# Kernel tuning notes

Measured on AMD Instinct MI355X. Metric: run time of the kernel, lower is better.

The kernel has to match this reference:

```python
import jax, jax.numpy as jnp
import numpy as np

G = 128            # grid_size (hardcoded in NeRFRenderer.__init__)
T = 32             # time_size (reduced from 64 to keep working set < 4GB)
CAS = 1            # cascade = 1 + ceil(log2(bound)), bound = 1
DECAY = 0.95
DENSITY_SCALE = 1.0
DENSITY_THRESH = 0.01


def _expand_bits(v):
    # instant-ngp style 10-bit -> 30-bit expansion (works for 7-bit coords of G=128)
    v = (v * jnp.uint32(0x00010001)) & jnp.uint32(0xFF0000FF)
    v = (v * jnp.uint32(0x00000101)) & jnp.uint32(0x0F00F00F)
    v = (v * jnp.uint32(0x00000011)) & jnp.uint32(0xC30C30C3)
    v = (v * jnp.uint32(0x00000005)) & jnp.uint32(0x49249249)
    return v


def _morton3d(coords):
    # coords: [N, 3] int32 in [0, G)
    x = _expand_bits(coords[:, 0].astype(jnp.uint32))
    y = _expand_bits(coords[:, 1].astype(jnp.uint32))
    z = _expand_bits(coords[:, 2].astype(jnp.uint32))
    return (x | (y << 1) | (z << 2)).astype(jnp.int32)


def setup_inputs() -> dict:
    key = jax.random.key(0)
    k1, k2 = jax.random.split(key)
    density_grid = jax.random.normal(k1, (T, CAS, G ** 3), dtype=jnp.float32) * 0.5
    sigmas = jax.random.uniform(k2, (T, CAS, G ** 3), dtype=jnp.float32)
    return {"density_grid": density_grid, "sigmas": sigmas}


def reference(density_grid, sigmas):
    # full-grid branch of update_extra_state (iter_density < 16)
    g = jnp.arange(G, dtype=jnp.int32)
    xx, yy, zz = jnp.meshgrid(g, g, g, indexing='ij')
    coords = jnp.stack([xx.ravel(), yy.ravel(), zz.ravel()], axis=-1)  # [G^3, 3]
    indices = _morton3d(coords)                                        # [G^3]

    # tmp_grid = -1; tmp_grid[t, cas, indices] = sigmas * density_scale
    tmp_grid = -jnp.ones_like(density_grid)
    tmp_grid = tmp_grid.at[:, :, indices].set(sigmas * DENSITY_SCALE)

    # decay / max merge on mutually-valid cells
    valid = (density_grid >= 0) & (tmp_grid >= 0)
    new_grid = jnp.where(valid, jnp.maximum(density_grid * DECAY, tmp_grid), density_grid)

    # threshold + packbits into bitfield (8 cells per byte, morton order)
    mean_density = jnp.mean(jnp.clip(new_grid, 0.0))
    thresh = jnp.minimum(mean_density, jnp.float32(DENSITY_THRESH))
    bits = (new_grid > thresh).reshape(T, -1, 8)                       # [T, CAS*G^3/8, 8]
    weights = (jnp.int32(1) << jnp.arange(8, dtype=jnp.int32))
    bitfield = jnp.sum(bits.astype(jnp.int32) * weights, axis=-1)      # [T, CAS*G^3/8]
    return new_grid, bitfield
```

## Files before the change

kernel.cpp:

```cpp
#include <hip/hip_runtime.h>

#define G    128
#define G3   (G * G * G)
#define TDIM 32
#define NTOT (TDIM * G3)
#define NBYTES_OUT (NTOT / 8)
#define DECAY 0.95f
#define DTH   0.01f
#define NBLK  (TDIM * 256)

typedef float f32x4 __attribute__((ext_vector_type(4)));
typedef float f32x2 __attribute__((ext_vector_type(2)));

__device__ __forceinline__ unsigned expand3(unsigned v) {
    v = (v * 0x00010001u) & 0xFF0000FFu;
    v = (v * 0x00000101u) & 0x0F00F00Fu;
    v = (v * 0x00000011u) & 0xC30C30C3u;
    v = (v * 0x00000005u) & 0x49249249u;
    return v;
}

__device__ __forceinline__ int swz(int f) {
    return f ^ ((((f >> 12) & 1) << 3) ^ (((f >> 8) & 1) << 4));
}

__device__ __forceinline__ f32x4 merge4(f32x4 v, f32x4 s) {
    f32x4 r;
    r.x = (v.x >= 0.f && s.x >= 0.f) ? fmaxf(v.x * DECAY, s.x) : v.x;
    r.y = (v.y >= 0.f && s.y >= 0.f) ? fmaxf(v.y * DECAY, s.y) : v.y;
    r.z = (v.z >= 0.f && s.z >= 0.f) ? fmaxf(v.z * DECAY, s.z) : v.z;
    r.w = (v.w >= 0.f && s.w >= 0.f) ? fmaxf(v.w * DECAY, s.w) : v.w;
    return r;
}

__global__ __launch_bounds__(512, 8) void
pass1(const float* __restrict__ dg, const float* __restrict__ sg,
      float* __restrict__ out_grid, float* __restrict__ out_bits,
      float* __restrict__ partials)
{
    __shared__ float smem[8192];
    __shared__ float wsum[8];
    const int blk  = blockIdx.x;
    const int t    = blk >> 8;
    const int pp   = blk & 255;
    const int sx   = pp & 15;
    const int sy   = pp >> 4;
    const int base = t * G3;
    const int tid  = threadIdx.x;

    const int m_fixed = (int)((expand3((unsigned)sx) << 9) | (expand3((unsigned)sy) << 10));
    const int r   = tid >> 5;
    const int o   = (tid & 31) << 4;
    const int jg0 = base + m_fixed + (int)(expand3((unsigned)r) << 11) + o;

    const f32x4* dgp = reinterpret_cast<const f32x4*>(dg + jg0);
    const f32x4 v0 = dgp[0];
    const f32x4 v1 = dgp[1];
    const f32x4 v2 = dgp[2];
    const f32x4 v3 = dgp[3];

    const float* __restrict__ sgt = sg + base + (sx << 17) + (sy << 10);
    #pragma unroll
    for (int k = 0; k < 4; ++k) {
        const int c   = tid + (k << 9);
        const int x   = c >> 8;
        const int rem = c & 255;
        const f32x4 s = *reinterpret_cast<const f32x4*>(sgt + (x << 14) + (rem << 2));
        *reinterpret_cast<f32x4*>(&smem[swz((x << 10) + (rem << 2))]) = s;
    }
    __syncthreads();

    const int lb = tid & 31;
    const int y1 = lb & 1, z1 = (lb >> 1) & 1, x2 = (lb >> 2) & 1;
    const int y2 = (lb >> 3) & 1, z2 = (lb >> 4) & 1;
    const int zz = (z1 << 1) + (z2 << 2) + (r << 3);

    f32x2 p0, p1, p2, p3, p4, p5, p6, p7;
    {
        const int xA = 2 * 0 + 4 * x2;
        const int xB = 2 * 1 + 4 * x2;
        const int yA = 2 * y1 + 4 * y2;
        const int fA = (xA << 10) + (yA << 7) + zz;
        const int fB = (xB << 10) + (yA << 7) + zz;
        p0 = *reinterpret_cast<const f32x2*>(&smem[swz(fA)]);
        p1 = *reinterpret_cast<const f32x2*>(&smem[swz(fA + 1024)]);
        p2 = *reinterpret_cast<const f32x2*>(&smem[swz(fA + 128)]);
        p3 = *reinterpret_cast<const f32x2*>(&smem[swz(fA + 1152)]);
        p4 = *reinterpret_cast<const f32x2*>(&smem[swz(fB)]);
        p5 = *reinterpret_cast<const f32x2*>(&smem[swz(fB + 1024)]);
        p6 = *reinterpret_cast<const f32x2*>(&smem[swz(fB + 128)]);
        p7 = *reinterpret_cast<const f32x2*>(&smem[swz(fB + 1152)]);
    }
    f32x4 s0; s0.x = p0.x; s0.y = p1.x; s0.z = p2.x; s0.w = p3.x;
    f32x4 s1; s1.x = p0.y; s1.y = p1.y; s1.z = p2.y; s1.w = p3.y;
    f32x4 s2; s2.x = p4.x; s2.y = p5.x; s2.z = p6.x; s2.w = p7.x;
    f32x4 s3; s3.x = p4.y; s3.y = p5.y; s3.z = p6.y; s3.w = p7.y;

    const f32x4 r0 = merge4(v0, s0);
    const f32x4 r1 = merge4(v1, s1);
    const f32x4 r2 = merge4(v2, s2);
    const f32x4 r3 = merge4(v3, s3);

    f32x4* ogp = reinterpret_cast<f32x4*>(out_grid + jg0);
    ogp[0] = r0;
    ogp[1] = r1;
    ogp[2] = r2;
    ogp[3] = r3;

    float lsum = fmaxf(r0.x, 0.f) + fmaxf(r0.y, 0.f) + fmaxf(r0.z, 0.f) + fmaxf(r0.w, 0.f)
               + fmaxf(r1.x, 0.f) + fmaxf(r1.y, 0.f) + fmaxf(r1.z, 0.f) + fmaxf(r1.w, 0.f)
               + fmaxf(r2.x, 0.f) + fmaxf(r2.y, 0.f) + fmaxf(r2.z, 0.f) + fmaxf(r2.w, 0.f)
               + fmaxf(r3.x, 0.f) + fmaxf(r3.y, 0.f) + fmaxf(r3.z, 0.f) + fmaxf(r3.w, 0.f);

    const int byte0 = (r0.x > DTH ? 1 : 0)  | (r0.y > DTH ? 2 : 0)  |
                      (r0.z > DTH ? 4 : 0)  | (r0.w > DTH ? 8 : 0)  |
                      (r1.x > DTH ? 16 : 0) | (r1.y > DTH ? 32 : 0) |
                      (r1.z > DTH ? 64 : 0) | (r1.w > DTH ? 128 : 0);
    const int byte1 = (r2.x > DTH ? 1 : 0)  | (r2.y > DTH ? 2 : 0)  |
                      (r2.z > DTH ? 4 : 0)  | (r2.w > DTH ? 8 : 0)  |
                      (r3.x > DTH ? 16 : 0) | (r3.y > DTH ? 32 : 0) |
                      (r3.z > DTH ? 64 : 0) | (r3.w > DTH ? 128 : 0);
    f32x2 bb; bb.x = (float)byte0; bb.y = (float)byte1;
    *reinterpret_cast<f32x2*>(out_bits + (jg0 >> 3)) = bb;

    #pragma unroll
    for (int offl = 32; offl; offl >>= 1) lsum += __shfl_down(lsum, offl, 64);
    if ((tid & 63) == 0) wsum[tid >> 6] = lsum;
    __syncthreads();
    if (tid == 0) {
        float tot = 0.f;
        #pragma unroll
        for (int i = 0; i < 8; ++i) tot += wsum[i];
        partials[blk] = tot;
    }
}

__global__ __launch_bounds__(1024) void
reduce_thresh(const float* __restrict__ partials, float* __restrict__ thresh)
{
    float s = 0.f;
    for (int i = threadIdx.x; i < NBLK; i += 1024) s += partials[i];
    #pragma unroll
    for (int off = 32; off; off >>= 1) s += __shfl_down(s, off, 64);
    __shared__ float wsum[16];
    if ((threadIdx.x & 63) == 0) wsum[threadIdx.x >> 6] = s;
    __syncthreads();
    if (threadIdx.x == 0) {
        float tot = 0.f;
        #pragma unroll
        for (int i = 0; i < 16; ++i) tot += wsum[i];
        thresh[0] = fminf(tot / (float)NTOT, DTH);
    }
}

__global__ __launch_bounds__(256) void
fix_bits(const float* __restrict__ grid, const float* __restrict__ thresh,
         float* __restrict__ out_bits)
{
    const float th = thresh[0];
    if (th == DTH) return;
    for (int n = blockIdx.x * 256 + threadIdx.x; n < NBYTES_OUT; n += 256 * 1024) {
        const float4* g = reinterpret_cast<const float4*>(grid) + (n << 1);
        const float4 a = g[0], b = g[1];
        int byte = (a.x > th ? 1 : 0)   | (a.y > th ? 2 : 0)   |
                   (a.z > th ? 4 : 0)   | (a.w > th ? 8 : 0)   |
                   (b.x > th ? 16 : 0)  | (b.y > th ? 32 : 0)  |
                   (b.z > th ? 64 : 0)  | (b.w > th ? 128 : 0);
        out_bits[n] = (float)byte;
    }
}

extern "C" void kernel_launch(void* const* d_in, const int* in_sizes, int n_in,
                              void* d_out, int out_size, void* d_ws, size_t ws_size,
                              hipStream_t stream)
{
    const float* dg = (const float*)d_in[0];
    const float* sg = (const float*)d_in[1];
    float* out_grid = (float*)d_out;
    float* out_bits = out_grid + NTOT;
    float* partials = (float*)d_ws;
    float* thresh   = partials + NBLK;

    pass1<<<NBLK, 512, 0, stream>>>(dg, sg, out_grid, out_bits, partials);
    reduce_thresh<<<1, 1024, 0, stream>>>(partials, thresh);
    fix_bits<<<1024, 256, 0, stream>>>(out_grid, thresh, out_bits);
}
```

Baseline: 160.8 us.

## Remap thread-to-cell assignment for coalesced grid access and conflict-free LDS reads

Each thread now handles four 16-byte chunks spaced 64/512/576 vectors apart instead of four contiguous vectors, so each wavefront's global loads and stores of the grid cover contiguous 1KB runs. The LDS swizzle and the gather of sigmas from shared memory are reworked to match, using scalar loads chosen to avoid bank conflicts. Bitfield bytes are built from nibbles exchanged between lane pairs with a shuffle, and only even lanes write them. The cost is extra shuffles, more scalar LDS reads and half the lanes idle during the bitfield store.

```diff
diff --git a/kernel.cpp b/kernel.cpp
--- a/kernel.cpp
+++ b/kernel.cpp
@@ -21,7 +21,7 @@
 }
 
 __device__ __forceinline__ int swz(int f) {
-    return f ^ ((((f >> 12) & 1) << 3) ^ (((f >> 8) & 1) << 4));
+    return f ^ ((((f >> 11) & 1) << 2) | (((f >> 8) & 1) << 3) | (((f >> 12) & 1) << 4));
 }
 
 __device__ __forceinline__ f32x4 merge4(f32x4 v, f32x4 s) {
@@ -47,17 +47,17 @@
     const int sy   = pp >> 4;
     const int base = t * G3;
     const int tid  = threadIdx.x;
+    const int w    = tid >> 6;
+    const int i    = tid & 63;
 
     const int m_fixed = (int)((expand3((unsigned)sx) << 9) | (expand3((unsigned)sy) << 10));
-    const int r   = tid >> 5;
-    const int o   = (tid & 31) << 4;
-    const int jg0 = base + m_fixed + (int)(expand3((unsigned)r) << 11) + o;
+    const int jgA = base + m_fixed + ((int)expand3((unsigned)w) << 14) + (i << 2);
 
-    const f32x4* dgp = reinterpret_cast<const f32x4*>(dg + jg0);
+    const f32x4* dgp = reinterpret_cast<const f32x4*>(dg + jgA);
     const f32x4 v0 = dgp[0];
-    const f32x4 v1 = dgp[1];
-    const f32x4 v2 = dgp[2];
-    const f32x4 v3 = dgp[3];
+    const f32x4 v1 = dgp[64];
+    const f32x4 v2 = dgp[512];
+    const f32x4 v3 = dgp[576];
 
     const float* __restrict__ sgt = sg + base + (sx << 17) + (sy << 10);
     #pragma unroll
@@ -70,58 +70,50 @@
     }
     __syncthreads();
 
-    const int lb = tid & 31;
-    const int y1 = lb & 1, z1 = (lb >> 1) & 1, x2 = (lb >> 2) & 1;
-    const int y2 = (lb >> 3) & 1, z2 = (lb >> 4) & 1;
-    const int zz = (z1 << 1) + (z2 << 2) + (r << 3);
-
-    f32x2 p0, p1, p2, p3, p4, p5, p6, p7;
-    {
-        const int xA = 2 * 0 + 4 * x2;
-        const int xB = 2 * 1 + 4 * x2;
-        const int yA = 2 * y1 + 4 * y2;
-        const int fA = (xA << 10) + (yA << 7) + zz;
-        const int fB = (xB << 10) + (yA << 7) + zz;
-        p0 = *reinterpret_cast<const f32x2*>(&smem[swz(fA)]);
-        p1 = *reinterpret_cast<const f32x2*>(&smem[swz(fA + 1024)]);
-        p2 = *reinterpret_cast<const f32x2*>(&smem[swz(fA + 128)]);
-        p3 = *reinterpret_cast<const f32x2*>(&smem[swz(fA + 1152)]);
-        p4 = *reinterpret_cast<const f32x2*>(&smem[swz(fB)]);
-        p5 = *reinterpret_cast<const f32x2*>(&smem[swz(fB + 1024)]);
-        p6 = *reinterpret_cast<const f32x2*>(&smem[swz(fB + 128)]);
-        p7 = *reinterpret_cast<const f32x2*>(&smem[swz(fB + 1152)]);
-    }
-    f32x4 s0; s0.x = p0.x; s0.y = p1.x; s0.z = p2.x; s0.w = p3.x;
-    f32x4 s1; s1.x = p0.y; s1.y = p1.y; s1.z = p2.y; s1.w = p3.y;
-    f32x4 s2; s2.x = p4.x; s2.y = p5.x; s2.z = p6.x; s2.w = p7.x;
-    f32x4 s3; s3.x = p4.y; s3.y = p5.y; s3.z = p6.y; s3.w = p7.y;
+    const int fi = (i & 1) | (((i >> 3) & 1) << 1) | (((i >> 2) & 1) << 8)
+                 | (((i >> 5) & 1) << 9) | (((i >> 1) & 1) << 11) | (((i >> 4) & 1) << 12);
+    const int S  = (((fi >> 11) & 1) << 2) | (((fi >> 8) & 1) << 3) | (((fi >> 12) & 1) << 4);
+    const int A  = w << 4;
+    const float* sp0 = &smem[fi | ((A + 0)  ^ S)];
+    const float* sp1 = &smem[fi | ((A + 4)  ^ S)];
+    const float* sp2 = &smem[fi | ((A + 8)  ^ S)];
+    const float* sp3 = &smem[fi | ((A + 12) ^ S)];
+    f32x4 s0; s0.x = sp0[0]; s0.y = sp0[1024]; s0.z = sp0[128]; s0.w = sp0[1152];
+    f32x4 s1; s1.x = sp1[0]; s1.y = sp1[1024]; s1.z = sp1[128]; s1.w = sp1[1152];
+    f32x4 s2; s2.x = sp2[0]; s2.y = sp2[1024]; s2.z = sp2[128]; s2.w = sp2[1152];
+    f32x4 s3; s3.x = sp3[0]; s3.y = sp3[1024]; s3.z = sp3[128]; s3.w = sp3[1152];
 
     const f32x4 r0 = merge4(v0, s0);
     const f32x4 r1 = merge4(v1, s1);
     const f32x4 r2 = merge4(v2, s2);
     const f32x4 r3 = merge4(v3, s3);
 
-    f32x4* ogp = reinterpret_cast<f32x4*>(out_grid + jg0);
-    ogp[0] = r0;
-    ogp[1] = r1;
-    ogp[2] = r2;
-    ogp[3] = r3;
+    f32x4* ogp = reinterpret_cast<f32x4*>(out_grid + jgA);
+    ogp[0]   = r0;
+    ogp[64]  = r1;
+    ogp[512] = r2;
+    ogp[576] = r3;
 
     float lsum = fmaxf(r0.x, 0.f) + fmaxf(r0.y, 0.f) + fmaxf(r0.z, 0.f) + fmaxf(r0.w, 0.f)
                + fmaxf(r1.x, 0.f) + fmaxf(r1.y, 0.f) + fmaxf(r1.z, 0.f) + fmaxf(r1.w, 0.f)
                + fmaxf(r2.x, 0.f) + fmaxf(r2.y, 0.f) + fmaxf(r2.z, 0.f) + fmaxf(r2.w, 0.f)
                + fmaxf(r3.x, 0.f) + fmaxf(r3.y, 0.f) + fmaxf(r3.z, 0.f) + fmaxf(r3.w, 0.f);
 
-    const int byte0 = (r0.x > DTH ? 1 : 0)  | (r0.y > DTH ? 2 : 0)  |
-                      (r0.z > DTH ? 4 : 0)  | (r0.w > DTH ? 8 : 0)  |
-                      (r1.x > DTH ? 16 : 0) | (r1.y > DTH ? 32 : 0) |
-                      (r1.z > DTH ? 64 : 0) | (r1.w > DTH ? 128 : 0);
-    const int byte1 = (r2.x > DTH ? 1 : 0)  | (r2.y > DTH ? 2 : 0)  |
-                      (r2.z > DTH ? 4 : 0)  | (r2.w > DTH ? 8 : 0)  |
-                      (r3.x > DTH ? 16 : 0) | (r3.y > DTH ? 32 : 0) |
-                      (r3.z > DTH ? 64 : 0) | (r3.w > DTH ? 128 : 0);
-    f32x2 bb; bb.x = (float)byte0; bb.y = (float)byte1;
-    *reinterpret_cast<f32x2*>(out_bits + (jg0 >> 3)) = bb;
+    int n0 = (r0.x > DTH ? 1 : 0) | (r0.y > DTH ? 2 : 0) | (r0.z > DTH ? 4 : 0) | (r0.w > DTH ? 8 : 0);
+    int n1 = (r1.x > DTH ? 1 : 0) | (r1.y > DTH ? 2 : 0) | (r1.z > DTH ? 4 : 0) | (r1.w > DTH ? 8 : 0);
+    int n2 = (r2.x > DTH ? 1 : 0) | (r2.y > DTH ? 2 : 0) | (r2.z > DTH ? 4 : 0) | (r2.w > DTH ? 8 : 0);
+    int n3 = (r3.x > DTH ? 1 : 0) | (r3.y > DTH ? 2 : 0) | (r3.z > DTH ? 4 : 0) | (r3.w > DTH ? 8 : 0);
+    const int p0 = __shfl_xor(n0, 1, 64);
+    const int p1 = __shfl_xor(n1, 1, 64);
+    const int p2 = __shfl_xor(n2, 1, 64);
+    const int p3 = __shfl_xor(n3, 1, 64);
+    if ((i & 1) == 0) {
+        float* bp = out_bits + (jgA >> 3);
+        bp[0]   = (float)(n0 | (p0 << 4));
+        bp[32]  = (float)(n1 | (p1 << 4));
+        bp[256] = (float)(n2 | (p2 << 4));
+        bp[288] = (float)(n3 | (p3 << 4));
+    }
 
     #pragma unroll
     for (int offl = 32; offl; offl >>= 1) lsum += __shfl_down(lsum, offl, 64);
@@ -130,7 +122,7 @@
     if (tid == 0) {
         float tot = 0.f;
         #pragma unroll
-        for (int i = 0; i < 8; ++i) tot += wsum[i];
+        for (int k = 0; k < 8; ++k) tot += wsum[k];
         partials[blk] = tot;
     }
 }
```

Measured after the change: 158.2 us. About the same (-1.6%).
